# Optimization experiments

Measured on AMD Instinct MI355X. Metric: run time of the kernel, lower is better.

Reference implementation:

```python
import jax, jax.numpy as jnp
import numpy as np

B, S, DIN, DQK, DV = 4, 4096, 1024, 64, 64


def setup_inputs() -> dict:
    key = jax.random.key(0)
    ks = jax.random.split(key, 10)
    inv = 1.0 / np.sqrt(DIN)
    return {
        "query": jax.random.normal(ks[0], (B, S, DIN), dtype=jnp.float32),
        "key": jax.random.normal(ks[1], (B, S, DIN), dtype=jnp.float32),
        "value": jax.random.normal(ks[2], (B, S, DIN), dtype=jnp.float32),
        "mask": jnp.ones((B, S, S), dtype=jnp.int32),
        "Wq": jax.random.uniform(ks[3], (DIN, DQK), jnp.float32, -inv, inv),
        "bq": jax.random.uniform(ks[4], (DQK,), jnp.float32, -inv, inv),
        "Wk": jax.random.uniform(ks[5], (DIN, DQK), jnp.float32, -inv, inv),
        "bk": jax.random.uniform(ks[6], (DQK,), jnp.float32, -inv, inv),
        "Wv": jax.random.uniform(ks[7], (DIN, DV), jnp.float32, -inv, inv),
        "bv": jax.random.uniform(ks[8], (DV,), jnp.float32, -inv, inv),
    }


def reference(query, key, value, mask, Wq, bq, Wk, bk, Wv, bv):
    q = jnp.einsum("bsd,de->bse", query, Wq) + bq  # [B,S,DQK]
    k = jnp.einsum("bsd,de->bse", key, Wk) + bk    # [B,S,DQK]
    v = jnp.einsum("bsd,de->bse", value, Wv) + bv  # [B,S,DV]
    # faithful nonstandard scale: sqrt(dim_qk + 1e-8)
    scale = jnp.sqrt(jnp.float32(q.shape[-1]) + 1e-8)
    scores = jnp.einsum("bqe,bke->bqk", q, k) / scale  # [B,S,S]
    scores = jnp.where(mask == 0, jnp.float32(-jnp.inf), scores)
    attn = jax.nn.softmax(scores, axis=-1)
    return jnp.einsum("bqk,bkv->bqv", attn, v)  # [B,S,DV]
```

## Files before the change

kernel.cpp:

```cpp
#include <hip/hip_runtime.h>

#define NB 4
#define NS 4096
#define NDIN 1024
#define ND 64

typedef __attribute__((ext_vector_type(4))) float f32x4;
typedef __attribute__((ext_vector_type(8))) short s16x8;
typedef __attribute__((ext_vector_type(4))) short s16x4;

__device__ __forceinline__ unsigned short f2bf(float f) {
  union { float f; unsigned u; } x; x.f = f;
  unsigned r = x.u + 0x7fffu + ((x.u >> 16) & 1u);
  return (unsigned short)(r >> 16);
}

__device__ __forceinline__ unsigned cvtpk(float lo, float hi) {
  unsigned r;
  asm("v_cvt_pk_bf16_f32 %0, %1, %2" : "=v"(r) : "v"(lo), "v"(hi));
  return r;
}

__device__ __forceinline__ void gload16(const void* g, void* l) {
  __builtin_amdgcn_global_load_lds(
      (const __attribute__((address_space(1))) void*)g,
      (__attribute__((address_space(3))) void*)l, 16, 0, 0);
}

__global__ __launch_bounds__(256) void prep_w_kernel(
    const float* __restrict__ Wq, const float* __restrict__ Wk,
    const float* __restrict__ Wv, unsigned short* __restrict__ wt) {
  int idx = blockIdx.x * 256 + threadIdx.x;
  int m = idx >> 16;
  int r = idx & 65535;
  int c = r >> 10;
  int k = r & 1023;
  const float* W = (m == 0) ? Wq : (m == 1) ? Wk : Wv;
  wt[idx] = f2bf(W[k * ND + c]);
}

__global__ __launch_bounds__(256, 3) void proj_kernel(
    const float* __restrict__ Xq, const float* __restrict__ Xk, const float* __restrict__ Xv,
    const float* __restrict__ bq, const float* __restrict__ bk, const float* __restrict__ bv,
    const unsigned short* __restrict__ wt_all,
    unsigned short* __restrict__ q_o, unsigned short* __restrict__ k_o,
    unsigned short* __restrict__ vt_o) {
  __shared__ float xsm[2][4096];
  __shared__ unsigned short wsm[2][4096];

  const int y = blockIdx.y;
  const float* __restrict__ X = (y == 0) ? Xq : (y == 1) ? Xk : Xv;
  const float* __restrict__ bias = (y == 0) ? bq : (y == 1) ? bk : bv;
  const char* __restrict__ wg = (const char*)(wt_all + y * (ND * NDIN));
  const int row0 = blockIdx.x * 64;
  const int tid = threadIdx.x;
  const int lane = tid & 63;
  const int w = tid >> 6;
  const int ql = lane & 15;
  const int grp = lane >> 4;
  const int swz = (ql & 7) << 4;

  int osrcX[4];
  #pragma unroll
  for (int j = 0; j < 4; ++j) {
    const int o = w * 4096 + j * 1024 + lane * 16;
    const int row = o >> 8, c = o & 255;
    osrcX[j] = row * 4096 + (c ^ ((row & 7) << 4));
  }
  int osrcW[2];
  #pragma unroll
  for (int j = 0; j < 2; ++j) {
    const int o = w * 2048 + j * 1024 + lane * 16;
    const int row = o >> 7, c = o & 127;
    osrcW[j] = row * 2048 + (c ^ ((row & 7) << 4));
  }

  const char* xg = (const char*)(X + (size_t)row0 * NDIN);
  auto stageX = [&](int kk, int buf) {
    const char* src = xg + kk * 256;
    char* dst = (char*)xsm + buf * 16384 + w * 4096;
    #pragma unroll
    for (int j = 0; j < 4; ++j) gload16(src + osrcX[j], dst + j * 1024);
  };
  auto stageW = [&](int kk, int buf) {
    const char* src = wg + kk * 128;
    char* dst = (char*)wsm + buf * 8192 + w * 2048;
    gload16(src + osrcW[0], dst);
    gload16(src + osrcW[1], dst + 1024);
  };

  const int fw0 = (grp * 16) ^ swz;
  const int fw1 = (grp * 16 + 64) ^ swz;

  f32x4 acc[4] = {};

  stageX(0, 0);
  stageW(0, 0);
  asm volatile("s_waitcnt vmcnt(0)" ::: "memory");
  __syncthreads();

  for (int kk = 0; kk < 16; ++kk) {
    const int cur = kk & 1;
    if (kk < 15) {
      stageX(kk + 1, cur ^ 1);
      stageW(kk + 1, cur ^ 1);
    }
    __builtin_amdgcn_sched_barrier(0);

    const char* xr = (const char*)xsm + cur * 16384 + (16 * w + ql) * 256;
    const char* wr = (const char*)wsm + cur * 8192;
    #pragma unroll
    for (int half = 0; half < 2; ++half) {
      const f32x4 a0 = *reinterpret_cast<const f32x4*>(
          xr + ((half * 128 + grp * 32) ^ swz));
      const f32x4 a1 = *reinterpret_cast<const f32x4*>(
          xr + ((half * 128 + grp * 32 + 16) ^ swz));
      union { s16x8 v; unsigned u[4]; } a;
      a.u[0] = cvtpk(a0[0], a0[1]);
      a.u[1] = cvtpk(a0[2], a0[3]);
      a.u[2] = cvtpk(a1[0], a1[1]);
      a.u[3] = cvtpk(a1[2], a1[3]);
      const int fw = half ? fw1 : fw0;
      #pragma unroll
      for (int nt = 0; nt < 4; ++nt) {
        const s16x8 bfr = *reinterpret_cast<const s16x8*>(wr + (ql + 16 * nt) * 128 + fw);
        acc[nt] = __builtin_amdgcn_mfma_f32_16x16x32_bf16(a.v, bfr, acc[nt], 0, 0, 0);
      }
    }

    asm volatile("s_waitcnt vmcnt(0)" ::: "memory");
    __syncthreads();
  }

  const int b = row0 >> 12;
  const int s0 = row0 & 4095;
  #pragma unroll
  for (int nt = 0; nt < 4; ++nt) {
    const int col = ql + 16 * nt;
    const float bia = bias[col];
    #pragma unroll
    for (int r = 0; r < 4; ++r) {
      const int rr = 16 * w + grp * 4 + r;
      const unsigned short h = f2bf(acc[nt][r] + bia);
      if (y == 0) {
        q_o[(size_t)(row0 + rr) * ND + col] = h;
      } else if (y == 1) {
        k_o[(size_t)(row0 + rr) * ND + col] = h;
      } else {
        vt_o[(size_t)b * ND * NS + (size_t)col * NS + (s0 + rr)] = h;
      }
    }
  }
}

__global__ __launch_bounds__(256, 4) void attn_kernel(
    const unsigned short* __restrict__ qm, const unsigned short* __restrict__ km,
    const unsigned short* __restrict__ vt, const int* __restrict__ mask,
    float* __restrict__ opart, float* __restrict__ ml) {
  __shared__ unsigned short ksm[2][4096];
  __shared__ unsigned short vsm[2][4096];
  __shared__ unsigned short psm[4096];

  const int bid = blockIdx.x;
  const int combo = bid & 15;
  const int qblk = bid >> 4;
  const int b = combo >> 2;
  const int split = combo & 3;
  const int q0 = qblk * 64;
  const int kv00 = split * 1024;

  const int tid = threadIdx.x;
  const int lane = tid & 63;
  const int w = tid >> 6;
  const int ql = lane & 15;
  const int grp = lane >> 4;

  const int swz = (ql & 7) << 4;
  const int fK0 = ql * 128 + ((grp * 16) ^ swz);
  const int fK1 = ql * 128 + ((grp * 16 + 64) ^ swz);

  int oK0, oK1, oV0, oV1;
  {
    const int o0 = w * 2048 + lane * 16;
    const int o1 = o0 + 1024;
    oK0 = o0 ^ (((o0 >> 7) & 7) << 4);
    oK1 = o1 ^ (((o1 >> 7) & 7) << 4);
    const int d0 = o0 >> 7, c0 = o0 & 127;
    const int d1 = o1 >> 7, c1 = o1 & 127;
    oV0 = d0 * 8192 + (c0 ^ ((d0 & 7) << 4));
    oV1 = d1 * 8192 + (c1 ^ ((d1 & 7) << 4));
  }

  const char* kg = (const char*)(km + (size_t)b * NS * ND + (size_t)kv00 * ND);
  const char* vg = (const char*)(vt + (size_t)b * ND * NS + kv00);
  char* const klds = (char*)&ksm[0][0] + w * 2048;
  char* const vlds = (char*)&vsm[0][0] + w * 2048;
  char* const pw = (char*)&psm[0] + w * 2048;

  const size_t qrow = (size_t)(b * NS + q0 + w * 16 + ql) * ND;
  const s16x8 qf0 = *reinterpret_cast<const s16x8*>(qm + qrow + grp * 8);
  const s16x8 qf1 = *reinterpret_cast<const s16x8*>(qm + qrow + 32 + grp * 8);

  const int* __restrict__ mrow =
      mask + (size_t)(b * NS + q0 + w * 16 + ql) * NS + kv00;

  f32x4 acc[4] = {};
  float m_i = -INFINITY;
  float l_i = 0.f;
  const float CSC = 0.18033688011112042f;
  const float THR = 11.54f;

  auto stage = [&](int t, int buf) {
    const char* kt = kg + (size_t)t * 8192;
    const char* vtb = vg + (size_t)t * 128;
    gload16(kt + oK0, klds + buf * 8192);
    gload16(kt + oK1, klds + buf * 8192 + 1024);
    gload16(vtb + oV0, vlds + buf * 8192);
    gload16(vtb + oV1, vlds + buf * 8192 + 1024);
  };

  int4 mcA[4], mcB[4];

  auto mload = [&](int4 (&m)[4], int tau) {
    const int* mn = mrow + tau * 64;
    m[0] = *reinterpret_cast<const int4*>(mn + grp * 4);
    m[1] = *reinterpret_cast<const int4*>(mn + 16 + grp * 4);
    m[2] = *reinterpret_cast<const int4*>(mn + 32 + grp * 4);
    m[3] = *reinterpret_cast<const int4*>(mn + 48 + grp * 4);
  };

  auto qk_apply = [&](const char* kread, const int4 (&m)[4], float (&sc)[16]) {
    f32x4 s4[4];
    __builtin_amdgcn_s_setprio(1);
    #pragma unroll
    for (int mt = 0; mt < 4; ++mt) {
      const s16x8 kf0 = *reinterpret_cast<const s16x8*>(kread + mt * 2048 + fK0);
      const s16x8 kf1 = *reinterpret_cast<const s16x8*>(kread + mt * 2048 + fK1);
      f32x4 s = {0.f, 0.f, 0.f, 0.f};
      s = __builtin_amdgcn_mfma_f32_16x16x32_bf16(kf0, qf0, s, 0, 0, 0);
      s = __builtin_amdgcn_mfma_f32_16x16x32_bf16(kf1, qf1, s, 0, 0, 0);
      s4[mt] = s;
    }
    __builtin_amdgcn_s_setprio(0);
    #pragma unroll
    for (int mt = 0; mt < 4; ++mt) {
      sc[4 * mt + 0] = (m[mt].x != 0) ? s4[mt][0] * CSC : -1e30f;
      sc[4 * mt + 1] = (m[mt].y != 0) ? s4[mt][1] * CSC : -1e30f;
      sc[4 * mt + 2] = (m[mt].z != 0) ? s4[mt][2] * CSC : -1e30f;
      sc[4 * mt + 3] = (m[mt].w != 0) ? s4[mt][3] * CSC : -1e30f;
    }
  };

  auto finish = [&](const char* vread, float (&sc)[16]) {
    float t0 = fmaxf(fmaxf(sc[0], sc[1]), fmaxf(sc[2], sc[3]));
    float t1 = fmaxf(fmaxf(sc[4], sc[5]), fmaxf(sc[6], sc[7]));
    float t2 = fmaxf(fmaxf(sc[8], sc[9]), fmaxf(sc[10], sc[11]));
    float t3 = fmaxf(fmaxf(sc[12], sc[13]), fmaxf(sc[14], sc[15]));
    const float tm = fmaxf(fmaxf(t0, t1), fmaxf(t2, t3));
    if (!__all(tm <= m_i + THR)) {
      float tw = fmaxf(tm, __shfl_xor(tm, 16));
      tw = fmaxf(tw, __shfl_xor(tw, 32));
      const float nm = fmaxf(m_i, tw);
      const float alpha = exp2f(m_i - nm);
      #pragma unroll
      for (int r = 0; r < 4; ++r) {
        const float ar = __shfl(alpha, grp * 4 + r);
        acc[0][r] *= ar;
        acc[1][r] *= ar;
        acc[2][r] *= ar;
        acc[3][r] *= ar;
      }
      l_i *= alpha;
      m_i = nm;
    }
    #pragma unroll
    for (int r = 0; r < 16; ++r) sc[r] = exp2f(sc[r] - m_i);
    float u0 = (sc[0] + sc[1]) + (sc[2] + sc[3]);
    float u1 = (sc[4] + sc[5]) + (sc[6] + sc[7]);
    float u2 = (sc[8] + sc[9]) + (sc[10] + sc[11]);
    float u3 = (sc[12] + sc[13]) + (sc[14] + sc[15]);
    l_i += (u0 + u1) + (u2 + u3);

    #pragma unroll
    for (int mt = 0; mt < 4; ++mt) {
      uint2 pk;
      pk.x = cvtpk(sc[4 * mt + 0], sc[4 * mt + 1]);
      pk.y = cvtpk(sc[4 * mt + 2], sc[4 * mt + 3]);
      *reinterpret_cast<uint2*>(pw + ql * 128 + ((mt * 32 + grp * 8) ^ swz)) = pk;
    }
    #pragma unroll
    for (int ks = 0; ks < 2; ++ks) {
      const s16x8 pa = *reinterpret_cast<const s16x8*>(
          pw + ql * 128 + ((ks * 64 + grp * 16) ^ swz));
      const int fV = ks ? fK1 : fK0;
      __builtin_amdgcn_s_setprio(1);
      #pragma unroll
      for (int nt = 0; nt < 4; ++nt) {
        const s16x8 vb = *reinterpret_cast<const s16x8*>(vread + nt * 2048 + fV);
        acc[nt] = __builtin_amdgcn_mfma_f32_16x16x32_bf16(pa, vb, acc[nt], 0, 0, 0);
      }
      __builtin_amdgcn_s_setprio(0);
    }
  };

  const char* const kbuf0 = (const char*)&ksm[0][0];
  const char* const kbuf1 = (const char*)&ksm[0][0] + 8192;
  const char* const vbuf0 = (const char*)&vsm[0][0];
  const char* const vbuf1 = (const char*)&vsm[0][0] + 8192;

  stage(0, 0);
  mload(mcB, 0);
  asm volatile("s_waitcnt vmcnt(0)" ::: "memory");
  __syncthreads();

  for (int tt = 0; tt < 14; tt += 2) {
    float sc[16];
    stage(tt + 1, 1);
    __builtin_amdgcn_sched_barrier(0);
    qk_apply(kbuf0, mcB, sc);
    mload(mcA, tt + 1);
    mload(mcB, tt + 2);
    __builtin_amdgcn_sched_barrier(0);
    finish(vbuf0, sc);
    asm volatile("s_waitcnt vmcnt(8)" ::: "memory");
    __builtin_amdgcn_s_barrier();

    float sd[16];
    stage(tt + 2, 0);
    __builtin_amdgcn_sched_barrier(0);
    qk_apply(kbuf1, mcA, sd);
    __builtin_amdgcn_sched_barrier(0);
    finish(vbuf1, sd);
    asm volatile("s_waitcnt vmcnt(0)" ::: "memory");
    __builtin_amdgcn_s_barrier();
  }

  {
    float sc[16];
    stage(15, 1);
    __builtin_amdgcn_sched_barrier(0);
    qk_apply(kbuf0, mcB, sc);
    mload(mcA, 15);
    __builtin_amdgcn_sched_barrier(0);
    finish(vbuf0, sc);
    asm volatile("s_waitcnt vmcnt(4)" ::: "memory");
    __builtin_amdgcn_s_barrier();
  }
  {
    float sc[16];
    qk_apply(kbuf1, mcA, sc);
    finish(vbuf1, sc);
  }

  float lq = l_i + __shfl_xor(l_i, 16);
  lq += __shfl_xor(lq, 32);

  const int qg = b * NS + q0 + w * 16;
  float* obase = opart + ((size_t)split * (NB * NS) + qg) * 64;
  #pragma unroll
  for (int nt = 0; nt < 4; ++nt) {
    #pragma unroll
    for (int r = 0; r < 4; ++r) {
      obase[(size_t)(grp * 4 + r) * 64 + ql + 16 * nt] = acc[nt][r];
    }
  }
  if (grp == 0) {
    float* mlp = ml + ((size_t)split * (NB * NS) + qg + ql) * 2;
    mlp[0] = m_i;
    mlp[1] = lq;
  }
}

__global__ __launch_bounds__(256) void combine_kernel(
    const float* __restrict__ opart, const float* __restrict__ ml,
    float* __restrict__ out) {
  const int idx = blockIdx.x * 256 + threadIdx.x;
  const int q = idx >> 4;
  const int dc = (idx & 15) * 4;
  const float2 a0 = *reinterpret_cast<const float2*>(ml + (size_t)q * 2);
  const float2 a1 = *reinterpret_cast<const float2*>(ml + (size_t)(16384 + q) * 2);
  const float2 a2 = *reinterpret_cast<const float2*>(ml + (size_t)(32768 + q) * 2);
  const float2 a3 = *reinterpret_cast<const float2*>(ml + (size_t)(49152 + q) * 2);
  const float M = fmaxf(fmaxf(a0.x, a1.x), fmaxf(a2.x, a3.x));
  const float w0 = exp2f(a0.x - M), w1 = exp2f(a1.x - M);
  const float w2 = exp2f(a2.x - M), w3 = exp2f(a3.x - M);
  const float inv = 1.f / (a0.y * w0 + a1.y * w1 + a2.y * w2 + a3.y * w3);
  f32x4 o = (*reinterpret_cast<const f32x4*>(opart + (size_t)q * 64 + dc)) * w0;
  o += (*reinterpret_cast<const f32x4*>(opart + ((size_t)16384 + q) * 64 + dc)) * w1;
  o += (*reinterpret_cast<const f32x4*>(opart + ((size_t)32768 + q) * 64 + dc)) * w2;
  o += (*reinterpret_cast<const f32x4*>(opart + ((size_t)49152 + q) * 64 + dc)) * w3;
  o *= inv;
  *reinterpret_cast<f32x4*>(out + (size_t)q * 64 + dc) = o;
}

extern "C" void kernel_launch(void* const* d_in, const int* in_sizes, int n_in,
                              void* d_out, int out_size, void* d_ws, size_t ws_size,
                              hipStream_t stream) {
  const float* query = (const float*)d_in[0];
  const float* key   = (const float*)d_in[1];
  const float* value = (const float*)d_in[2];
  const int*   mask  = (const int*)d_in[3];
  const float* Wq = (const float*)d_in[4];
  const float* bq = (const float*)d_in[5];
  const float* Wk = (const float*)d_in[6];
  const float* bk = (const float*)d_in[7];
  const float* Wv = (const float*)d_in[8];
  const float* bv = (const float*)d_in[9];
  float* out = (float*)d_out;

  char* ws = (char*)d_ws;
  unsigned short* wt    = (unsigned short*)(ws);
  unsigned short* qb    = (unsigned short*)(ws + 393216);
  unsigned short* kb    = (unsigned short*)(ws + 2490368);
  unsigned short* vtb   = (unsigned short*)(ws + 4587520);
  float*          opart = (float*)(ws + 6684672);
  float*          mlb   = (float*)(ws + 23461888);

  prep_w_kernel<<<dim3(768), dim3(256), 0, stream>>>(Wq, Wk, Wv, wt);
  proj_kernel<<<dim3(256, 3), dim3(256), 0, stream>>>(query, key, value,
                                                      bq, bk, bv, wt, qb, kb, vtb);
  attn_kernel<<<dim3(1024), dim3(256), 0, stream>>>(qb, kb, vtb, mask, opart, mlb);
  combine_kernel<<<dim3(1024), dim3(256), 0, stream>>>(opart, mlb, out);
}
```

Measured before the change: 125.8 us.

## Halve KV split count and burst-prefetch mask tiles four at a time

The attention kernel now splits the key range into 2 chunks of 2048 instead of 4 of 1024, so it launches 512 blocks and each processes 32 KV tiles. Mask rows are loaded in bursts covering four tiles into double-buffered register arrays, and the loop is restructured into four-tile windows with full __syncthreads between stages in place of the hand-tuned vmcnt waits. The combine kernel merges only two partials, cutting partial-output traffic. In exchange, 512 blocks on 256 CUs gives less parallelism and latency hiding, the launch bound drops to 2 blocks per CU, and the larger mask register buffers raise register pressure.

```diff
diff --git a/kernel.cpp b/kernel.cpp
--- a/kernel.cpp
+++ b/kernel.cpp
@@ -153,7 +153,7 @@
   }
 }
 
-__global__ __launch_bounds__(256, 4) void attn_kernel(
+__global__ __launch_bounds__(256, 2) void attn_kernel(
     const unsigned short* __restrict__ qm, const unsigned short* __restrict__ km,
     const unsigned short* __restrict__ vt, const int* __restrict__ mask,
     float* __restrict__ opart, float* __restrict__ ml) {
@@ -162,12 +162,12 @@
   __shared__ unsigned short psm[4096];
 
   const int bid = blockIdx.x;
-  const int combo = bid & 15;
-  const int qblk = bid >> 4;
-  const int b = combo >> 2;
-  const int split = combo & 3;
+  const int combo = bid & 7;
+  const int qblk = bid >> 3;
+  const int b = combo >> 1;
+  const int split = combo & 1;
   const int q0 = qblk * 64;
-  const int kv00 = split * 1024;
+  const int kv00 = split * 2048;
 
   const int tid = threadIdx.x;
   const int lane = tid & 63;
@@ -219,17 +219,18 @@
     gload16(vtb + oV1, vlds + buf * 8192 + 1024);
   };
 
-  int4 mcA[4], mcB[4];
-
-  auto mload = [&](int4 (&m)[4], int tau) {
-    const int* mn = mrow + tau * 64;
-    m[0] = *reinterpret_cast<const int4*>(mn + grp * 4);
-    m[1] = *reinterpret_cast<const int4*>(mn + 16 + grp * 4);
-    m[2] = *reinterpret_cast<const int4*>(mn + 32 + grp * 4);
-    m[3] = *reinterpret_cast<const int4*>(mn + 48 + grp * 4);
-  };
-
-  auto qk_apply = [&](const char* kread, const int4 (&m)[4], float (&sc)[16]) {
+  auto mburst = [&](int4 (&dst)[4][4], int tau) {
+    #pragma unroll
+    for (int i = 0; i < 4; ++i) {
+      const int* mp = mrow + (tau + i) * 64 + grp * 4;
+      dst[i][0] = *reinterpret_cast<const int4*>(mp);
+      dst[i][1] = *reinterpret_cast<const int4*>(mp + 16);
+      dst[i][2] = *reinterpret_cast<const int4*>(mp + 32);
+      dst[i][3] = *reinterpret_cast<const int4*>(mp + 48);
+    }
+  };
+
+  auto body = [&](const char* kread, const char* vread, const int4 (&m)[4]) {
     f32x4 s4[4];
     __builtin_amdgcn_s_setprio(1);
     #pragma unroll
@@ -242,6 +243,8 @@
       s4[mt] = s;
     }
     __builtin_amdgcn_s_setprio(0);
+
+    float sc[16];
     #pragma unroll
     for (int mt = 0; mt < 4; ++mt) {
       sc[4 * mt + 0] = (m[mt].x != 0) ? s4[mt][0] * CSC : -1e30f;
@@ -249,9 +252,7 @@
       sc[4 * mt + 2] = (m[mt].z != 0) ? s4[mt][2] * CSC : -1e30f;
       sc[4 * mt + 3] = (m[mt].w != 0) ? s4[mt][3] * CSC : -1e30f;
     }
-  };
-
-  auto finish = [&](const char* vread, float (&sc)[16]) {
+
     float t0 = fmaxf(fmaxf(sc[0], sc[1]), fmaxf(sc[2], sc[3]));
     float t1 = fmaxf(fmaxf(sc[4], sc[5]), fmaxf(sc[6], sc[7]));
     float t2 = fmaxf(fmaxf(sc[8], sc[9]), fmaxf(sc[10], sc[11]));
@@ -308,48 +309,41 @@
   const char* const vbuf0 = (const char*)&vsm[0][0];
   const char* const vbuf1 = (const char*)&vsm[0][0] + 8192;
 
+  int4 MA[4][4], MB[4][4];
+
   stage(0, 0);
-  mload(mcB, 0);
+  mburst(MA, 0);
   asm volatile("s_waitcnt vmcnt(0)" ::: "memory");
   __syncthreads();
 
-  for (int tt = 0; tt < 14; tt += 2) {
-    float sc[16];
-    stage(tt + 1, 1);
+  auto window = [&](int W, const int4 (&cur)[4][4], int4 (&nxt)[4][4]) {
+    const int T = 4 * W;
+    stage(T + 1, 1);
+    if (W < 7) mburst(nxt, T + 4);
     __builtin_amdgcn_sched_barrier(0);
-    qk_apply(kbuf0, mcB, sc);
-    mload(mcA, tt + 1);
-    mload(mcB, tt + 2);
+    body(kbuf0, vbuf0, cur[0]);
+    __syncthreads();
+    stage(T + 2, 0);
     __builtin_amdgcn_sched_barrier(0);
-    finish(vbuf0, sc);
-    asm volatile("s_waitcnt vmcnt(8)" ::: "memory");
-    __builtin_amdgcn_s_barrier();
-
-    float sd[16];
-    stage(tt + 2, 0);
+    body(kbuf1, vbuf1, cur[1]);
+    __syncthreads();
+    stage(T + 3, 1);
     __builtin_amdgcn_sched_barrier(0);
-    qk_apply(kbuf1, mcA, sd);
-    __builtin_amdgcn_sched_barrier(0);
-    finish(vbuf1, sd);
-    asm volatile("s_waitcnt vmcnt(0)" ::: "memory");
-    __builtin_amdgcn_s_barrier();
-  }
-
-  {
-    float sc[16];
-    stage(15, 1);
-    __builtin_amdgcn_sched_barrier(0);
-    qk_apply(kbuf0, mcB, sc);
-    mload(mcA, 15);
-    __builtin_amdgcn_sched_barrier(0);
-    finish(vbuf0, sc);
-    asm volatile("s_waitcnt vmcnt(4)" ::: "memory");
-    __builtin_amdgcn_s_barrier();
-  }
-  {
-    float sc[16];
-    qk_apply(kbuf1, mcA, sc);
-    finish(vbuf1, sc);
+    body(kbuf0, vbuf0, cur[2]);
+    __syncthreads();
+    if (T + 4 < 32) {
+      stage(T + 4, 0);
+      __builtin_amdgcn_sched_barrier(0);
+      body(kbuf1, vbuf1, cur[3]);
+      __syncthreads();
+    } else {
+      body(kbuf1, vbuf1, cur[3]);
+    }
+  };
+
+  for (int WW = 0; WW < 8; WW += 2) {
+    window(WW, MA, MB);
+    window(WW + 1, MB, MA);
   }
 
   float lq = l_i + __shfl_xor(l_i, 16);
@@ -379,16 +373,11 @@
   const int dc = (idx & 15) * 4;
   const float2 a0 = *reinterpret_cast<const float2*>(ml + (size_t)q * 2);
   const float2 a1 = *reinterpret_cast<const float2*>(ml + (size_t)(16384 + q) * 2);
-  const float2 a2 = *reinterpret_cast<const float2*>(ml + (size_t)(32768 + q) * 2);
-  const float2 a3 = *reinterpret_cast<const float2*>(ml + (size_t)(49152 + q) * 2);
-  const float M = fmaxf(fmaxf(a0.x, a1.x), fmaxf(a2.x, a3.x));
+  const float M = fmaxf(a0.x, a1.x);
   const float w0 = exp2f(a0.x - M), w1 = exp2f(a1.x - M);
-  const float w2 = exp2f(a2.x - M), w3 = exp2f(a3.x - M);
-  const float inv = 1.f / (a0.y * w0 + a1.y * w1 + a2.y * w2 + a3.y * w3);
+  const float inv = 1.f / (a0.y * w0 + a1.y * w1);
   f32x4 o = (*reinterpret_cast<const f32x4*>(opart + (size_t)q * 64 + dc)) * w0;
   o += (*reinterpret_cast<const f32x4*>(opart + ((size_t)16384 + q) * 64 + dc)) * w1;
-  o += (*reinterpret_cast<const f32x4*>(opart + ((size_t)32768 + q) * 64 + dc)) * w2;
-  o += (*reinterpret_cast<const f32x4*>(opart + ((size_t)49152 + q) * 64 + dc)) * w3;
   o *= inv;
   *reinterpret_cast<f32x4*>(out + (size_t)q * 64 + dc) = o;
 }
@@ -419,6 +408,6 @@
   prep_w_kernel<<<dim3(768), dim3(256), 0, stream>>>(Wq, Wk, Wv, wt);
   proj_kernel<<<dim3(256, 3), dim3(256), 0, stream>>>(query, key, value,
                                                       bq, bk, bv, wt, qb, kb, vtb);
-  attn_kernel<<<dim3(1024), dim3(256), 0, stream>>>(qb, kb, vtb, mask, opart, mlb);
+  attn_kernel<<<dim3(512), dim3(256), 0, stream>>>(qb, kb, vtb, mask, opart, mlb);
   combine_kernel<<<dim3(1024), dim3(256), 0, stream>>>(opart, mlb, out);
 }
```

Measured after the change: 131.6 us. 4.6% more time.
